# Optimization experiments

Measured on AMD Instinct MI355X. Metric: run time of the kernel, lower is better.

## Reference

```python
import jax, jax.numpy as jnp
import numpy as np


def setup_inputs() -> dict:
    key = jax.random.key(0)
    k1, k2, k3 = jax.random.split(key, 3)
    B, S, D, E, H = 4, 2048, 1024, 8, 1024
    x = jax.random.normal(k1, (B, S, D), dtype=jnp.float32)
    Wg = jax.random.normal(k2, (D, E), dtype=jnp.float32) / np.sqrt(D)
    We = jax.random.normal(k3, (E, D, H), dtype=jnp.float32) / np.sqrt(D)
    be = jnp.zeros((E, H), dtype=jnp.float32)
    return {"x": x, "Wg": Wg, "We": We, "be": be}


def reference(x, Wg, We, be):
    B, S, D = x.shape
    E = Wg.shape[1]
    T = B * S
    xf = x.reshape(T, D)
    # Top-2 gating (softmax over experts, renormalize the chosen 2)
    gates = jax.nn.softmax(xf @ Wg, axis=-1)                 # [T, E]
    top_g, top_i = jax.lax.top_k(gates, 2)                   # [T, 2]
    top_g = top_g / jnp.sum(top_g, axis=-1, keepdims=True)
    # Dense dispatch matrix: dispatch[e, t] = combined gate weight of token t for expert e
    tok = jnp.arange(T)
    dispatch = jnp.zeros((E, T), dtype=gates.dtype)
    for i in range(2):  # fixed top-2, not a data loop
        dispatch = dispatch.at[top_i[:, i], tok].add(top_g[:, i])
    # Per-expert linear (grouped GEMM over all tokens), then weighted combine
    y = jnp.einsum('td,edh->eth', xf, We) + be[:, None, :]   # [E, T, H]
    out = jnp.einsum('et,eth->th', dispatch, y)              # [T, H]
    return out.reshape(B, S, -1)
```

## Files before the change

kernel.cpp:

```cpp
#include <hip/hip_runtime.h>
#include <hip/hip_bf16.h>

#define T_TOK 8192
#define DDIM  1024
#define NEXP  8
#define HDIM  1024
#define SLOT_CAP 17536
#define NCBLK 32

typedef short bf16x8 __attribute__((ext_vector_type(8)));
typedef float f32x4  __attribute__((ext_vector_type(4)));
typedef unsigned short u16x8 __attribute__((ext_vector_type(8)));

typedef const __attribute__((address_space(1))) unsigned int* gas_ptr;
typedef __attribute__((address_space(3))) unsigned int*       las_ptr;
#define GLD16(gp, lp) __builtin_amdgcn_global_load_lds((gas_ptr)(gp), (las_ptr)(lp), 16, 0, 0)

static __device__ __forceinline__ unsigned short f2b(float f) {
    union { float f; unsigned int u; } v; v.f = f;
    unsigned int u = v.u;
    u += 0x7fffu + ((u >> 16) & 1u);
    return (unsigned short)(u >> 16);
}
static __device__ __forceinline__ float b2f(unsigned short h) {
    union { unsigned int u; float f; } v; v.u = ((unsigned int)h) << 16;
    return v.f;
}

__global__ __launch_bounds__(256) void moe_routing(
    const float* __restrict__ x, const float* __restrict__ wg,
    unsigned short* __restrict__ xb,
    int* __restrict__ tok_e, float* __restrict__ tok_g)
{
    int wv   = threadIdx.x >> 6;
    int lane = threadIdx.x & 63;
    int t    = blockIdx.x * 4 + wv;

    const float4* xr = (const float4*)(x + (size_t)t * DDIM);
    float4 v[4];
    #pragma unroll
    for (int i = 0; i < 4; i++) v[i] = xr[lane + 64 * i];

    ushort4* xw = (ushort4*)(xb + (size_t)t * DDIM);
    #pragma unroll
    for (int i = 0; i < 4; i++) {
        ushort4 s4;
        s4.x = f2b(v[i].x); s4.y = f2b(v[i].y);
        s4.z = f2b(v[i].z); s4.w = f2b(v[i].w);
        xw[lane + 64 * i] = s4;
    }

    double s[NEXP];
    #pragma unroll
    for (int e = 0; e < NEXP; e++) s[e] = 0.0;
    #pragma unroll
    for (int i = 0; i < 4; i++) {
        const float* wr = wg + ((size_t)lane * 4 + 256 * i) * NEXP;
        #pragma unroll
        for (int j = 0; j < 4; j++) {
            double xj = (double)((&v[i].x)[j]);
            #pragma unroll
            for (int e = 0; e < NEXP; e++)
                s[e] += xj * (double)wr[j * NEXP + e];
        }
    }

    #pragma unroll
    for (int off = 32; off > 0; off >>= 1) {
        #pragma unroll
        for (int e = 0; e < NEXP; e++)
            s[e] += __shfl_xor(s[e], off, 64);
    }

    if (lane == 0) {
        int e0 = 0;
        for (int e = 1; e < NEXP; e++) if (s[e] > s[e0]) e0 = e;
        int e1 = (e0 == 0) ? 1 : 0;
        for (int e = 0; e < NEXP; e++) if (e != e0 && s[e] > s[e1]) e1 = e;
        double g0 = 1.0 / (1.0 + exp(s[e1] - s[e0]));
        tok_e[2*t] = e0; tok_e[2*t+1] = e1;
        tok_g[2*t] = (float)g0; tok_g[2*t+1] = (float)(1.0 - g0);
    }
}

__global__ __launch_bounds__(256) void moe_count(
    const int* __restrict__ tok_e, int* __restrict__ cnt_part)
{
    __shared__ int h[NEXP];
    if (threadIdx.x < NEXP) h[threadIdx.x] = 0;
    __syncthreads();
    int t = blockIdx.x * 256 + threadIdx.x;
    atomicAdd(&h[tok_e[2*t]], 1);
    atomicAdd(&h[tok_e[2*t+1]], 1);
    __syncthreads();
    if (threadIdx.x < NEXP)
        cnt_part[blockIdx.x * NEXP + threadIdx.x] = h[threadIdx.x];
}

__global__ __launch_bounds__(256) void moe_slotfill(
    const int* __restrict__ tok_e, const int* __restrict__ cnt_part,
    int* __restrict__ meta, int* __restrict__ counts,
    int* __restrict__ slot_token, int* __restrict__ tok_slot)
{
    __shared__ int h[NEXP];
    __shared__ int tots[NEXP], pres[NEXP], base[NEXP];
    int tid = threadIdx.x;
    if (tid < NEXP) h[tid] = 0;
    __syncthreads();
    int t = blockIdx.x * 256 + tid;
    int e0 = tok_e[2*t],     e1 = tok_e[2*t + 1];
    int r0 = atomicAdd(&h[e0], 1);
    int r1 = atomicAdd(&h[e1], 1);
    if (tid < NEXP) {
        int pre = 0, tot = 0;
        for (int b = 0; b < NCBLK; b++) {
            int c = cnt_part[b * NEXP + tid];
            if (b < (int)blockIdx.x) pre += c;
            tot += c;
        }
        tots[tid] = tot; pres[tid] = pre;
    }
    __syncthreads();
    if (tid < NEXP) {
        int off = 0;
        for (int e = 0; e < tid; e++) off += (tots[e] + 127) & ~127;
        base[tid] = off + pres[tid];
        if (blockIdx.x == 0) {
            meta[tid]   = off;
            counts[tid] = tots[tid];
            if (tid == NEXP - 1) meta[NEXP] = off + ((tots[tid] + 127) & ~127);
        }
    }
    __syncthreads();
    int s0 = base[e0] + r0, s1 = base[e1] + r1;
    slot_token[s0] = t;  tok_slot[2*t]     = s0;
    slot_token[s1] = t;  tok_slot[2*t + 1] = s1;
}

__global__ __launch_bounds__(256) void moe_wtrans(
    const float* __restrict__ we, unsigned short* __restrict__ wt)
{
    __shared__ unsigned short tile[64][65];
    int e  = blockIdx.z;
    int d0 = blockIdx.y * 64;
    int h0 = blockIdx.x * 64;
    int c  = threadIdx.x & 63;
    int r4 = threadIdx.x >> 6;
    #pragma unroll
    for (int i = 0; i < 64; i += 4)
        tile[r4 + i][c] = f2b(we[((size_t)e * DDIM + d0 + r4 + i) * HDIM + h0 + c]);
    __syncthreads();
    #pragma unroll
    for (int i = 0; i < 64; i += 4)
        wt[((size_t)e * HDIM + h0 + r4 + i) * DDIM + d0 + c] = tile[c][r4 + i];
}

__global__ __launch_bounds__(256, 3) void moe_gemm(
    const unsigned short* __restrict__ xb,
    const unsigned short* __restrict__ wt,
    const float* __restrict__ be,
    const int* __restrict__ slot_token,
    const int* __restrict__ meta,
    const int* __restrict__ counts,
    unsigned short* __restrict__ y_slot)
{
    __shared__ __align__(16) unsigned short As[3][128 * 32];
    __shared__ __align__(16) unsigned short Bs[3][128 * 32];

    int f   = blockIdx.y * gridDim.x + blockIdx.x;
    int wid = (f & 7) * gridDim.y + (f >> 3);
    int m0 = (wid >> 3) * 128;
    if (m0 >= meta[NEXP]) return;
    int n0 = (wid & 7) * 128;

    int e = 0;
    #pragma unroll
    for (int i = 1; i < NEXP; i++) if (m0 >= meta[i]) e = i;
    int lim = meta[e] + counts[e];

    int tid  = threadIdx.x;
    int lane = tid & 63, wv = tid >> 6;

    int rA = 32 * wv + (lane >> 2);
    int kc = (((lane & 3) ^ ((rA >> 1) & 3)) * 8);
    int sA0 = m0 + rA, sA1 = sA0 + 16;
    int tA0 = (sA0 < lim) ? slot_token[sA0] : 0;
    int tA1 = (sA1 < lim) ? slot_token[sA1] : 0;
    const unsigned short* gA0 = xb + (size_t)tA0 * DDIM + kc;
    const unsigned short* gA1 = xb + (size_t)tA1 * DDIM + kc;
    const unsigned short* gB0 = wt + ((size_t)e * HDIM + n0 + rA) * DDIM + kc;
    const unsigned short* gB1 = gB0 + (size_t)16 * DDIM;
    int c0 = (2 * wv) * 512;
    int c1 = c0 + 512;

    f32x4 acc[4][4];
    #pragma unroll
    for (int i = 0; i < 4; i++)
        #pragma unroll
        for (int j = 0; j < 4; j++) acc[i][j] = (f32x4){0.f, 0.f, 0.f, 0.f};

    int wm = (wv >> 1) * 64, wn = (wv & 1) * 64;
    int l16 = lane & 15, quad = lane >> 4;
    int ff = (l16 >> 1) & 3;
    int rdA[4], rdB[4];
    #pragma unroll
    for (int i = 0; i < 4; i++) {
        rdA[i] = (wm + i * 16 + l16) * 32 + ((quad ^ ff) * 8);
        rdB[i] = (wn + i * 16 + l16) * 32 + ((quad ^ ff) * 8);
    }

#define ISSUE_A(kkv, Ab)                                                      \
    {                                                                         \
        int ko = (kkv) * 32;                                                  \
        GLD16(gA0 + ko, (Ab) + c0);                                           \
        GLD16(gA1 + ko, (Ab) + c1);                                           \
    }
#define ISSUE_B(kkv, Bb)                                                      \
    {                                                                         \
        int ko = (kkv) * 32;                                                  \
        GLD16(gB0 + ko, (Bb) + c0);                                           \
        GLD16(gB1 + ko, (Bb) + c1);                                           \
    }
#define COMPUTE(Ab, Bb)                                                       \
    {                                                                         \
        bf16x8 bfr[4];                                                        \
        _Pragma("unroll")                                                     \
        for (int j = 0; j < 4; j++)                                           \
            bfr[j] = *(const bf16x8*)((Bb) + rdB[j]);                         \
        _Pragma("unroll")                                                     \
        for (int i = 0; i < 4; i++) {                                         \
            bf16x8 af = *(const bf16x8*)((Ab) + rdA[i]);                      \
            _Pragma("unroll")                                                 \
            for (int j = 0; j < 4; j++)                                       \
                acc[i][j] = __builtin_amdgcn_mfma_f32_16x16x32_bf16(          \
                    af, bfr[j], acc[i][j], 0, 0, 0);                          \
        }                                                                     \
    }

    unsigned short *A0 = As[0], *A1 = As[1], *A2 = As[2];
    unsigned short *B0 = Bs[0], *B1 = Bs[1], *B2 = Bs[2];

    ISSUE_A(0, A0)
    ISSUE_B(0, B0)
    ISSUE_A(1, A1)
    ISSUE_B(1, B1)

    #pragma unroll 1
    for (int kk = 0; kk < 32; ++kk) {
        asm volatile("" ::: "memory");
        if (kk == 31) __builtin_amdgcn_s_waitcnt(0x0F70);
        else          __builtin_amdgcn_s_waitcnt(0x0F74);
        __builtin_amdgcn_s_barrier();
        asm volatile("" ::: "memory");
        if (kk < 30) {
            ISSUE_B(kk + 2, B2)
            ISSUE_A(kk + 2, A2)
        }
        COMPUTE(A0, B0)
        unsigned short* tA = A0; A0 = A1; A1 = A2; A2 = tA;
        unsigned short* tB = B0; B0 = B1; B1 = tB; tB = B1;
        B1 = B2; B2 = tB;
    }
#undef ISSUE_A
#undef ISSUE_B
#undef COMPUTE

    #pragma unroll
    for (int i = 0; i < 4; i++) {
        #pragma unroll
        for (int r = 0; r < 4; r++) {
            int slot = m0 + wm + i * 16 + quad * 4 + r;
            if (slot >= lim) continue;
            unsigned short* yp = y_slot + (size_t)slot * HDIM + n0;
            #pragma unroll
            for (int j = 0; j < 4; j++) {
                int col = wn + j * 16 + l16;
                yp[col] = f2b(acc[i][j][r] + be[e * HDIM + n0 + col]);
            }
        }
    }
}

__global__ __launch_bounds__(256) void moe_combine(
    const unsigned short* __restrict__ y_slot,
    const int* __restrict__ tok_slot, const float* __restrict__ tok_g,
    float* __restrict__ out)
{
    int tid  = threadIdx.x;
    int half = tid >> 7;
    int lane = tid & 127;
    int t = blockIdx.x * 2 + half;
    int s0 = tok_slot[2 * t], s1 = tok_slot[2 * t + 1];
    float g0 = tok_g[2 * t],  g1 = tok_g[2 * t + 1];
    u16x8 a = ((const u16x8*)(y_slot + (size_t)s0 * HDIM))[lane];
    u16x8 b = ((const u16x8*)(y_slot + (size_t)s1 * HDIM))[lane];
    float4 o0, o1;
    o0.x = g0 * b2f(a[0]) + g1 * b2f(b[0]);
    o0.y = g0 * b2f(a[1]) + g1 * b2f(b[1]);
    o0.z = g0 * b2f(a[2]) + g1 * b2f(b[2]);
    o0.w = g0 * b2f(a[3]) + g1 * b2f(b[3]);
    o1.x = g0 * b2f(a[4]) + g1 * b2f(b[4]);
    o1.y = g0 * b2f(a[5]) + g1 * b2f(b[5]);
    o1.z = g0 * b2f(a[6]) + g1 * b2f(b[6]);
    o1.w = g0 * b2f(a[7]) + g1 * b2f(b[7]);
    float4* op = (float4*)(out + (size_t)t * HDIM) + lane * 2;
    op[0] = o0;
    op[1] = o1;
}

extern "C" void kernel_launch(void* const* d_in, const int* in_sizes, int n_in,
                              void* d_out, int out_size, void* d_ws, size_t ws_size,
                              hipStream_t stream) {
    const float* x  = (const float*)d_in[0];
    const float* wg = (const float*)d_in[1];
    const float* we = (const float*)d_in[2];
    const float* be = (const float*)d_in[3];
    float* out = (float*)d_out;

    char* ws = (char*)d_ws;
    size_t o = 0;
    auto alloc = [&](size_t bytes) -> void* {
        void* p = ws + o;
        o = (o + bytes + 255) & ~(size_t)255;
        return p;
    };
    unsigned short* xb   = (unsigned short*)alloc((size_t)T_TOK * DDIM * 2);
    unsigned short* wtb  = (unsigned short*)alloc((size_t)NEXP * HDIM * DDIM * 2);
    unsigned short* ysl  = (unsigned short*)alloc((size_t)SLOT_CAP * HDIM * 2);
    int*   slot_token    = (int*)  alloc((size_t)SLOT_CAP * 4);
    int*   cnt_part      = (int*)  alloc((size_t)NCBLK * NEXP * 4);
    int*   counts        = (int*)  alloc(NEXP * 4);
    int*   meta          = (int*)  alloc((NEXP + 1) * 4);
    int*   tok_e         = (int*)  alloc((size_t)T_TOK * 2 * 4);
    float* tok_g         = (float*)alloc((size_t)T_TOK * 2 * 4);
    int*   tok_slot      = (int*)  alloc((size_t)T_TOK * 2 * 4);

    moe_routing<<<T_TOK / 4, 256, 0, stream>>>(x, wg, xb, tok_e, tok_g);
    moe_count<<<NCBLK, 256, 0, stream>>>(tok_e, cnt_part);
    moe_slotfill<<<NCBLK, 256, 0, stream>>>(tok_e, cnt_part, meta, counts,
                                            slot_token, tok_slot);
    moe_wtrans<<<dim3(HDIM / 64, DDIM / 64, NEXP), 256, 0, stream>>>(we, wtb);
    moe_gemm<<<dim3(HDIM / 128, SLOT_CAP / 128), 256, 0, stream>>>(
        xb, wtb, be, slot_token, meta, counts, ysl);
    moe_combine<<<T_TOK / 2, 256, 0, stream>>>(ysl, tok_slot, tok_g, out);
}
```

Measured before the change: 214.0 us.

## Enlarge grouped GEMM tile to 256x256 with 8 waves and 4-stage ping-pong pipeline

The expert GEMM moves from 128x128 tiles on 4 waves to 256x256 tiles on 8 waves, with a 4-deep LDS ring. Each k-step is split into two MFMA halves, with A and B staging interleaved between barriers and s_setprio raised around the MFMA bursts. Expert padding grows to 256 rows to match the larger M tile, and the slot capacity and grid are resized to fit. The aim is more data reuse per global load and better overlap of loads with MFMA work. The cost is more padded rows per expert, more barriers per k-step, more registers, and fewer blocks, which hurts tail balance.

New measurement: 230.1 us. 7.6% more time.

```diff
diff --git a/kernel.cpp b/kernel.cpp
--- a/kernel.cpp
+++ b/kernel.cpp
@@ -5,7 +5,7 @@
 #define DDIM  1024
 #define NEXP  8
 #define HDIM  1024
-#define SLOT_CAP 17536
+#define SLOT_CAP 18432
 #define NCBLK 32
 
 typedef short bf16x8 __attribute__((ext_vector_type(8)));
@@ -123,12 +123,12 @@
     __syncthreads();
     if (tid < NEXP) {
         int off = 0;
-        for (int e = 0; e < tid; e++) off += (tots[e] + 127) & ~127;
+        for (int e = 0; e < tid; e++) off += (tots[e] + 255) & ~255;
         base[tid] = off + pres[tid];
         if (blockIdx.x == 0) {
             meta[tid]   = off;
             counts[tid] = tots[tid];
-            if (tid == NEXP - 1) meta[NEXP] = off + ((tots[tid] + 127) & ~127);
+            if (tid == NEXP - 1) meta[NEXP] = off + ((tots[tid] + 255) & ~255);
         }
     }
     __syncthreads();
@@ -155,7 +155,7 @@
         wt[((size_t)e * HDIM + h0 + r4 + i) * DDIM + d0 + c] = tile[c][r4 + i];
 }
 
-__global__ __launch_bounds__(256, 3) void moe_gemm(
+__global__ __launch_bounds__(512, 2) void moe_gemm(
     const unsigned short* __restrict__ xb,
     const unsigned short* __restrict__ wt,
     const float* __restrict__ be,
@@ -164,14 +164,14 @@
     const int* __restrict__ counts,
     unsigned short* __restrict__ y_slot)
 {
-    __shared__ __align__(16) unsigned short As[3][128 * 32];
-    __shared__ __align__(16) unsigned short Bs[3][128 * 32];
+    __shared__ __align__(16) unsigned short As[4][256 * 32];
+    __shared__ __align__(16) unsigned short Bs[4][256 * 32];
 
     int f   = blockIdx.y * gridDim.x + blockIdx.x;
-    int wid = (f & 7) * gridDim.y + (f >> 3);
-    int m0 = (wid >> 3) * 128;
+    int wid = (f & 7) * 36 + (f >> 3);
+    int m0 = (wid >> 2) * 256;
     if (m0 >= meta[NEXP]) return;
-    int n0 = (wid & 7) * 128;
+    int n0 = (wid & 3) * 256;
 
     int e = 0;
     #pragma unroll
@@ -181,92 +181,104 @@
     int tid  = threadIdx.x;
     int lane = tid & 63, wv = tid >> 6;
 
-    int rA = 32 * wv + (lane >> 2);
-    int kc = (((lane & 3) ^ ((rA >> 1) & 3)) * 8);
-    int sA0 = m0 + rA, sA1 = sA0 + 16;
+    int rS  = 16 * wv + (lane >> 2);
+    int kc  = (((lane & 3) ^ ((rS >> 1) & 3)) * 8);
+    int c0  = wv * 512;
+    int c1  = 4096 + wv * 512;
+
+    int sA0 = m0 + rS, sA1 = sA0 + 128;
     int tA0 = (sA0 < lim) ? slot_token[sA0] : 0;
     int tA1 = (sA1 < lim) ? slot_token[sA1] : 0;
     const unsigned short* gA0 = xb + (size_t)tA0 * DDIM + kc;
     const unsigned short* gA1 = xb + (size_t)tA1 * DDIM + kc;
-    const unsigned short* gB0 = wt + ((size_t)e * HDIM + n0 + rA) * DDIM + kc;
-    const unsigned short* gB1 = gB0 + (size_t)16 * DDIM;
-    int c0 = (2 * wv) * 512;
-    int c1 = c0 + 512;
-
-    f32x4 acc[4][4];
-    #pragma unroll
-    for (int i = 0; i < 4; i++)
+    const unsigned short* gB0 = wt + ((size_t)e * HDIM + n0 + rS) * DDIM + kc;
+    const unsigned short* gB1 = gB0 + (size_t)128 * DDIM;
+
+    f32x4 acc[8][4];
+    #pragma unroll
+    for (int i = 0; i < 8; i++)
         #pragma unroll
         for (int j = 0; j < 4; j++) acc[i][j] = (f32x4){0.f, 0.f, 0.f, 0.f};
 
-    int wm = (wv >> 1) * 64, wn = (wv & 1) * 64;
+    int wm = (wv >> 2) * 128, wn = (wv & 3) * 64;
     int l16 = lane & 15, quad = lane >> 4;
     int ff = (l16 >> 1) & 3;
-    int rdA[4], rdB[4];
-    #pragma unroll
-    for (int i = 0; i < 4; i++) {
+    int rdA[8], rdB[4];
+    #pragma unroll
+    for (int i = 0; i < 8; i++)
         rdA[i] = (wm + i * 16 + l16) * 32 + ((quad ^ ff) * 8);
-        rdB[i] = (wn + i * 16 + l16) * 32 + ((quad ^ ff) * 8);
-    }
-
-#define ISSUE_A(kkv, Ab)                                                      \
+    #pragma unroll
+    for (int j = 0; j < 4; j++)
+        rdB[j] = (wn + j * 16 + l16) * 32 + ((quad ^ ff) * 8);
+
+#define STAGE_A(kt, Ab)                                                       \
     {                                                                         \
-        int ko = (kkv) * 32;                                                  \
+        int ko = (kt) * 32;                                                   \
         GLD16(gA0 + ko, (Ab) + c0);                                           \
         GLD16(gA1 + ko, (Ab) + c1);                                           \
     }
-#define ISSUE_B(kkv, Bb)                                                      \
+#define STAGE_B(kt, Bb)                                                       \
     {                                                                         \
-        int ko = (kkv) * 32;                                                  \
+        int ko = (kt) * 32;                                                   \
         GLD16(gB0 + ko, (Bb) + c0);                                           \
         GLD16(gB1 + ko, (Bb) + c1);                                           \
     }
-#define COMPUTE(Ab, Bb)                                                       \
-    {                                                                         \
-        bf16x8 bfr[4];                                                        \
-        _Pragma("unroll")                                                     \
-        for (int j = 0; j < 4; j++)                                           \
-            bfr[j] = *(const bf16x8*)((Bb) + rdB[j]);                         \
-        _Pragma("unroll")                                                     \
-        for (int i = 0; i < 4; i++) {                                         \
-            bf16x8 af = *(const bf16x8*)((Ab) + rdA[i]);                      \
-            _Pragma("unroll")                                                 \
-            for (int j = 0; j < 4; j++)                                       \
-                acc[i][j] = __builtin_amdgcn_mfma_f32_16x16x32_bf16(          \
-                    af, bfr[j], acc[i][j], 0, 0, 0);                          \
-        }                                                                     \
-    }
-
-    unsigned short *A0 = As[0], *A1 = As[1], *A2 = As[2];
-    unsigned short *B0 = Bs[0], *B1 = Bs[1], *B2 = Bs[2];
-
-    ISSUE_A(0, A0)
-    ISSUE_B(0, B0)
-    ISSUE_A(1, A1)
-    ISSUE_B(1, B1)
+
+    STAGE_A(0, As[0]) STAGE_B(0, Bs[0])
+    STAGE_A(1, As[1]) STAGE_B(1, Bs[1])
+    __builtin_amdgcn_s_waitcnt(0x0F74);
+    __builtin_amdgcn_s_barrier();
+    asm volatile("" ::: "memory");
 
     #pragma unroll 1
-    for (int kk = 0; kk < 32; ++kk) {
-        asm volatile("" ::: "memory");
-        if (kk == 31) __builtin_amdgcn_s_waitcnt(0x0F70);
-        else          __builtin_amdgcn_s_waitcnt(0x0F74);
+    for (int t = 0; t < 32; ++t) {
+        unsigned short* Ab = As[t & 3];
+        unsigned short* Bb = Bs[t & 3];
+        bf16x8 bfr[4];
+        #pragma unroll
+        for (int j = 0; j < 4; j++) bfr[j] = *(const bf16x8*)(Bb + rdB[j]);
+        bf16x8 afr[4];
+        #pragma unroll
+        for (int i = 0; i < 4; i++) afr[i] = *(const bf16x8*)(Ab + rdA[i]);
+        if (t < 30) STAGE_A(t + 2, As[(t + 2) & 3])
+        asm volatile("" ::: "memory");
         __builtin_amdgcn_s_barrier();
         asm volatile("" ::: "memory");
-        if (kk < 30) {
-            ISSUE_B(kk + 2, B2)
-            ISSUE_A(kk + 2, A2)
-        }
-        COMPUTE(A0, B0)
-        unsigned short* tA = A0; A0 = A1; A1 = A2; A2 = tA;
-        unsigned short* tB = B0; B0 = B1; B1 = tB; tB = B1;
-        B1 = B2; B2 = tB;
-    }
-#undef ISSUE_A
-#undef ISSUE_B
-#undef COMPUTE
-
-    #pragma unroll
-    for (int i = 0; i < 4; i++) {
+        __builtin_amdgcn_s_setprio(1);
+        #pragma unroll
+        for (int i = 0; i < 4; i++)
+            #pragma unroll
+            for (int j = 0; j < 4; j++)
+                acc[i][j] = __builtin_amdgcn_mfma_f32_16x16x32_bf16(
+                    afr[i], bfr[j], acc[i][j], 0, 0, 0);
+        __builtin_amdgcn_s_setprio(0);
+        asm volatile("" ::: "memory");
+        __builtin_amdgcn_s_barrier();
+        asm volatile("" ::: "memory");
+        #pragma unroll
+        for (int i = 0; i < 4; i++) afr[i] = *(const bf16x8*)(Ab + rdA[i + 4]);
+        if (t < 30) STAGE_B(t + 2, Bs[(t + 2) & 3])
+        asm volatile("" ::: "memory");
+        __builtin_amdgcn_s_barrier();
+        asm volatile("" ::: "memory");
+        __builtin_amdgcn_s_setprio(1);
+        #pragma unroll
+        for (int i = 0; i < 4; i++)
+            #pragma unroll
+            for (int j = 0; j < 4; j++)
+                acc[i + 4][j] = __builtin_amdgcn_mfma_f32_16x16x32_bf16(
+                    afr[i], bfr[j], acc[i + 4][j], 0, 0, 0);
+        __builtin_amdgcn_s_setprio(0);
+        if (t < 30) __builtin_amdgcn_s_waitcnt(0x0F74);
+        else        __builtin_amdgcn_s_waitcnt(0x0F70);
+        __builtin_amdgcn_s_barrier();
+        asm volatile("" ::: "memory");
+    }
+#undef STAGE_A
+#undef STAGE_B
+
+    #pragma unroll
+    for (int i = 0; i < 8; i++) {
         #pragma unroll
         for (int r = 0; r < 4; r++) {
             int slot = m0 + wm + i * 16 + quad * 4 + r;
@@ -340,7 +352,7 @@
     moe_slotfill<<<NCBLK, 256, 0, stream>>>(tok_e, cnt_part, meta, counts,
                                             slot_token, tok_slot);
     moe_wtrans<<<dim3(HDIM / 64, DDIM / 64, NEXP), 256, 0, stream>>>(we, wtb);
-    moe_gemm<<<dim3(HDIM / 128, SLOT_CAP / 128), 256, 0, stream>>>(
+    moe_gemm<<<dim3(HDIM / 256, SLOT_CAP / 256), 512, 0, stream>>>(
         xb, wtb, be, slot_token, meta, counts, ysl);
     moe_combine<<<T_TOK / 2, 256, 0, stream>>>(ysl, tok_slot, tok_g, out);
 }
```

## Enlarge GEMM block tile to 256x128 with 8 waves and raise MFMA priority

Applied to the files above, without the earlier changes.

The grouped GEMM moves from 128x128 tiles with 4 waves to 256x128 tiles with 8 waves (512 threads), so each B (weight) tile loaded into LDS serves twice as many token rows. To keep tiles aligned, expert segment padding changes from 128 to 256 slots and the slot capacity grows. The pipeline keeps three LDS stages, indexed by modulo instead of pointer rotation, and wraps the MFMA compute in s_setprio to favour math issue over loads. In exchange, more padding rows are computed per expert and each block uses more LDS, which may lower the number of resident blocks per CU.

Measured after the change: 222.8 us. +4.1%, slower.

```diff
diff --git a/kernel.cpp b/kernel.cpp
--- a/kernel.cpp
+++ b/kernel.cpp
@@ -5,7 +5,7 @@
 #define DDIM  1024
 #define NEXP  8
 #define HDIM  1024
-#define SLOT_CAP 17536
+#define SLOT_CAP 18432
 #define NCBLK 32
 
 typedef short bf16x8 __attribute__((ext_vector_type(8)));
@@ -123,12 +123,12 @@
     __syncthreads();
     if (tid < NEXP) {
         int off = 0;
-        for (int e = 0; e < tid; e++) off += (tots[e] + 127) & ~127;
+        for (int e = 0; e < tid; e++) off += (tots[e] + 255) & ~255;
         base[tid] = off + pres[tid];
         if (blockIdx.x == 0) {
             meta[tid]   = off;
             counts[tid] = tots[tid];
-            if (tid == NEXP - 1) meta[NEXP] = off + ((tots[tid] + 127) & ~127);
+            if (tid == NEXP - 1) meta[NEXP] = off + ((tots[tid] + 255) & ~255);
         }
     }
     __syncthreads();
@@ -155,7 +155,7 @@
         wt[((size_t)e * HDIM + h0 + r4 + i) * DDIM + d0 + c] = tile[c][r4 + i];
 }
 
-__global__ __launch_bounds__(256, 3) void moe_gemm(
+__global__ __launch_bounds__(512, 4) void moe_gemm(
     const unsigned short* __restrict__ xb,
     const unsigned short* __restrict__ wt,
     const float* __restrict__ be,
@@ -164,12 +164,12 @@
     const int* __restrict__ counts,
     unsigned short* __restrict__ y_slot)
 {
-    __shared__ __align__(16) unsigned short As[3][128 * 32];
+    __shared__ __align__(16) unsigned short As[3][256 * 32];
     __shared__ __align__(16) unsigned short Bs[3][128 * 32];
 
     int f   = blockIdx.y * gridDim.x + blockIdx.x;
-    int wid = (f & 7) * gridDim.y + (f >> 3);
-    int m0 = (wid >> 3) * 128;
+    int wid = (f & 7) * 72 + (f >> 3);
+    int m0 = (wid >> 3) * 256;
     if (m0 >= meta[NEXP]) return;
     int n0 = (wid & 7) * 128;
 
@@ -181,17 +181,17 @@
     int tid  = threadIdx.x;
     int lane = tid & 63, wv = tid >> 6;
 
-    int rA = 32 * wv + (lane >> 2);
-    int kc = (((lane & 3) ^ ((rA >> 1) & 3)) * 8);
-    int sA0 = m0 + rA, sA1 = sA0 + 16;
+    int rS  = 16 * wv + (lane >> 2);
+    int kc  = (((lane & 3) ^ ((rS >> 1) & 3)) * 8);
+    int c0  = wv * 512;
+    int c1  = 4096 + wv * 512;
+
+    int sA0 = m0 + rS, sA1 = sA0 + 128;
     int tA0 = (sA0 < lim) ? slot_token[sA0] : 0;
     int tA1 = (sA1 < lim) ? slot_token[sA1] : 0;
     const unsigned short* gA0 = xb + (size_t)tA0 * DDIM + kc;
     const unsigned short* gA1 = xb + (size_t)tA1 * DDIM + kc;
-    const unsigned short* gB0 = wt + ((size_t)e * HDIM + n0 + rA) * DDIM + kc;
-    const unsigned short* gB1 = gB0 + (size_t)16 * DDIM;
-    int c0 = (2 * wv) * 512;
-    int c1 = c0 + 512;
+    const unsigned short* gB0 = wt + ((size_t)e * HDIM + n0 + rS) * DDIM + kc;
 
     f32x4 acc[4][4];
     #pragma unroll
@@ -209,17 +209,12 @@
         rdB[i] = (wn + i * 16 + l16) * 32 + ((quad ^ ff) * 8);
     }
 
-#define ISSUE_A(kkv, Ab)                                                      \
+#define STAGE(kt, Ab, Bb)                                                     \
     {                                                                         \
-        int ko = (kkv) * 32;                                                  \
+        int ko = (kt) * 32;                                                   \
         GLD16(gA0 + ko, (Ab) + c0);                                           \
         GLD16(gA1 + ko, (Ab) + c1);                                           \
-    }
-#define ISSUE_B(kkv, Bb)                                                      \
-    {                                                                         \
-        int ko = (kkv) * 32;                                                  \
         GLD16(gB0 + ko, (Bb) + c0);                                           \
-        GLD16(gB1 + ko, (Bb) + c1);                                           \
     }
 #define COMPUTE(Ab, Bb)                                                       \
     {                                                                         \
@@ -237,32 +232,22 @@
         }                                                                     \
     }
 
-    unsigned short *A0 = As[0], *A1 = As[1], *A2 = As[2];
-    unsigned short *B0 = Bs[0], *B1 = Bs[1], *B2 = Bs[2];
-
-    ISSUE_A(0, A0)
-    ISSUE_B(0, B0)
-    ISSUE_A(1, A1)
-    ISSUE_B(1, B1)
+    STAGE(0, As[0], Bs[0])
+    STAGE(1, As[1], Bs[1])
 
     #pragma unroll 1
-    for (int kk = 0; kk < 32; ++kk) {
+    for (int t = 0; t < 32; ++t) {
         asm volatile("" ::: "memory");
-        if (kk == 31) __builtin_amdgcn_s_waitcnt(0x0F70);
-        else          __builtin_amdgcn_s_waitcnt(0x0F74);
+        if (t == 31) __builtin_amdgcn_s_waitcnt(0x0F70);
+        else         __builtin_amdgcn_s_waitcnt(0x0F73);
         __builtin_amdgcn_s_barrier();
         asm volatile("" ::: "memory");
-        if (kk < 30) {
-            ISSUE_B(kk + 2, B2)
-            ISSUE_A(kk + 2, A2)
-        }
-        COMPUTE(A0, B0)
-        unsigned short* tA = A0; A0 = A1; A1 = A2; A2 = tA;
-        unsigned short* tB = B0; B0 = B1; B1 = tB; tB = B1;
-        B1 = B2; B2 = tB;
-    }
-#undef ISSUE_A
-#undef ISSUE_B
+        if (t < 30) STAGE(t + 2, As[(t + 2) % 3], Bs[(t + 2) % 3])
+        __builtin_amdgcn_s_setprio(1);
+        COMPUTE(As[t % 3], Bs[t % 3])
+        __builtin_amdgcn_s_setprio(0);
+    }
+#undef STAGE
 #undef COMPUTE
 
     #pragma unroll
@@ -340,7 +325,7 @@
     moe_slotfill<<<NCBLK, 256, 0, stream>>>(tok_e, cnt_part, meta, counts,
                                             slot_token, tok_slot);
     moe_wtrans<<<dim3(HDIM / 64, DDIM / 64, NEXP), 256, 0, stream>>>(we, wtb);
-    moe_gemm<<<dim3(HDIM / 128, SLOT_CAP / 128), 256, 0, stream>>>(
+    moe_gemm<<<dim3(HDIM / 128, SLOT_CAP / 256), 512, 0, stream>>>(
         xb, wtb, be, slot_token, meta, counts, ysl);
     moe_combine<<<T_TOK / 2, 256, 0, stream>>>(ysl, tok_slot, tok_g, out);
 }
```
